# Kernel optimization log

Hardware: AMD Instinct MI355X
Metric: run time of the kernel (lower is better)

The kernel has to match this reference:

```python
import jax, jax.numpy as jnp
import numpy as np

N_NODES = 100000
IN_CH = 65
HID_CH = 64
N_EDGES = 3200000


def setup_inputs() -> dict:
    key = jax.random.key(0)
    k1, k2, k3, k4, k5 = jax.random.split(key, 5)
    x = jax.random.normal(k1, (N_NODES, IN_CH), dtype=jnp.float32)
    edge_index = jax.random.randint(k2, (2, N_EDGES), 0, N_NODES, dtype=jnp.int64)
    edge_weight = jax.random.uniform(k3, (N_EDGES,), dtype=jnp.float32)
    # PyG GraphConv params: lin_rel (with bias) applied to aggregated neighbors,
    # lin_root (no bias) applied to self features.
    scale = 1.0 / np.sqrt(IN_CH)
    W_rel = jax.random.uniform(k4, (HID_CH, IN_CH), dtype=jnp.float32, minval=-scale, maxval=scale)
    b_rel = jnp.zeros((HID_CH,), dtype=jnp.float32)
    W_root = jax.random.uniform(k5, (HID_CH, IN_CH), dtype=jnp.float32, minval=-scale, maxval=scale)
    return {"x": x, "edge_index": edge_index, "edge_weight": edge_weight,
            "W_rel": W_rel, "b_rel": b_rel, "W_root": W_root}


def reference(x, edge_index, edge_weight, W_rel, b_rel, W_root):
    src = edge_index[0]  # source nodes (x_j in PyG message)
    dst = edge_index[1]  # target nodes (aggregation index)
    # gather neighbor features, weight by edge weight: [E, IN_CH]
    msgs = x[src] * edge_weight[:, None]
    # scatter-add to destination nodes: [N, IN_CH]
    aggr = jax.ops.segment_sum(msgs, dst, num_segments=N_NODES)
    # out = lin_rel(aggr) + lin_root(x)
    out = aggr @ W_rel.T + b_rel + x @ W_root.T
    return out
```

## Files before the change

kernel.cpp:

```cpp
#include <hip/hip_runtime.h>

#define IN_CH 65
#define HID 64
#define BN 64
#define NB 1563
#define CAP 2560
#define SCAP 2432
#define EPB 12288
#define TPS 1024
#define EPT (EPB / TPS)
#define WSTR 132

static inline size_t align16(size_t v) { return (v + 15) & ~(size_t)15; }

__device__ inline ushort f2bf(float f) {
    uint u = __float_as_uint(f);
    return (ushort)((u + 0x7FFF + ((u >> 16) & 1)) >> 16);
}

__global__ __launch_bounds__(256) void k1both(const float* __restrict__ x,
                                              const float* __restrict__ W_rel,
                                              const float* __restrict__ W_root,
                                              const float* __restrict__ b_rel,
                                              ushort* __restrict__ y16,
                                              float* __restrict__ out,
                                              int* __restrict__ cnt, int nBuckets,
                                              int nNodes) {
    __shared__ float xsT[65 * 68];
    __shared__ float ws[65 * 68];
    const int tid = threadIdx.x;
    const int tx = tid & 15;
    const int ty = tid >> 4;
    const long nodeBase = (long)blockIdx.x * 64;
    const int nValid = (int)min((long)64, (long)nNodes - nodeBase);

    if (cnt && tid == 0 && blockIdx.x < (unsigned)nBuckets) cnt[blockIdx.x] = 0;

    for (int f = tid; f < HID * IN_CH; f += 256) {
        const int j = f / IN_CH, c = f - j * IN_CH;
        ws[c * 68 + j] = W_rel[f];
    }
    const float* xsrc = x + nodeBase * IN_CH;
    for (int f = tid; f < 64 * IN_CH; f += 256) {
        const int node = f / IN_CH, k = f - node * IN_CH;
        xsT[k * 68 + node] = (node < nValid) ? xsrc[f] : 0.f;
    }
    __syncthreads();

    const int r0 = ty * 4;
    const int c0 = tx * 4;

    {
        float acc[4][4];
#pragma unroll
        for (int i = 0; i < 4; ++i)
#pragma unroll
            for (int j = 0; j < 4; ++j) acc[i][j] = 0.f;

        for (int k = 0; k < IN_CH; ++k) {
            const float4 a4 = *(const float4*)&xsT[k * 68 + r0];
            const float4 b4 = *(const float4*)&ws[k * 68 + c0];
            const float aa[4] = {a4.x, a4.y, a4.z, a4.w};
            const float bb[4] = {b4.x, b4.y, b4.z, b4.w};
#pragma unroll
            for (int i = 0; i < 4; ++i)
#pragma unroll
                for (int j = 0; j < 4; ++j) acc[i][j] += aa[i] * bb[j];
        }
#pragma unroll
        for (int i = 0; i < 4; ++i) {
            const long node = nodeBase + r0 + i;
            if (node >= nNodes) break;
            uint2 pk;
            pk.x = (uint)f2bf(acc[i][0]) | ((uint)f2bf(acc[i][1]) << 16);
            pk.y = (uint)f2bf(acc[i][2]) | ((uint)f2bf(acc[i][3]) << 16);
            *(uint2*)&y16[node * HID + c0] = pk;
        }
    }
    __syncthreads();

    for (int f = tid; f < HID * IN_CH; f += 256) {
        const int j = f / IN_CH, c = f - j * IN_CH;
        ws[c * 68 + j] = W_root[f];
    }
    __syncthreads();

    {
        const float4 bb4 = *(const float4*)&b_rel[c0];
        float acc[4][4];
#pragma unroll
        for (int i = 0; i < 4; ++i) {
            acc[i][0] = bb4.x; acc[i][1] = bb4.y;
            acc[i][2] = bb4.z; acc[i][3] = bb4.w;
        }
        for (int k = 0; k < IN_CH; ++k) {
            const float4 a4 = *(const float4*)&xsT[k * 68 + r0];
            const float4 b4 = *(const float4*)&ws[k * 68 + c0];
            const float aa[4] = {a4.x, a4.y, a4.z, a4.w};
            const float bb[4] = {b4.x, b4.y, b4.z, b4.w};
#pragma unroll
            for (int i = 0; i < 4; ++i)
#pragma unroll
                for (int j = 0; j < 4; ++j) acc[i][j] += aa[i] * bb[j];
        }
#pragma unroll
        for (int i = 0; i < 4; ++i) {
            const long node = nodeBase + r0 + i;
            if (node >= nNodes) break;
            *(float4*)&out[node * HID + c0] =
                make_float4(acc[i][0], acc[i][1], acc[i][2], acc[i][3]);
        }
    }
}

__global__ __launch_bounds__(TPS) void scatterB(const int* __restrict__ ei,
                                                const float* __restrict__ ew,
                                                int* __restrict__ cnt,
                                                int2* __restrict__ pairs, int E) {
    __shared__ int lhist[NB];
    __shared__ int lbase[NB];
    const int tid = threadIdx.x;
    const long e0 = (long)blockIdx.x * EPB;
    const int n = (int)min((long)EPB, (long)E - e0);

    for (int i = tid; i < NB; i += TPS) lhist[i] = 0;
    __syncthreads();

    int dstv[EPT], srcv[EPT];
    float wv[EPT];
#pragma unroll
    for (int k = 0; k < EPT; ++k) {
        const int i = tid + k * TPS;
        const bool valid = i < n;
        dstv[k] = valid ? ei[(long)E + e0 + i] : 0;
        srcv[k] = valid ? ei[e0 + i] : 0;
        wv[k]   = valid ? ew[e0 + i] : 0.f;
        if (valid) atomicAdd(&lhist[dstv[k] >> 6], 1);
    }
    __syncthreads();

    for (int i = tid; i < NB; i += TPS) {
        const int c = lhist[i];
        lbase[i] = c ? atomicAdd(&cnt[i], c) : 0;
        lhist[i] = 0;
    }
    __syncthreads();

#pragma unroll
    for (int k = 0; k < EPT; ++k) {
        const int i = tid + k * TPS;
        if (i < n) {
            const int b = dstv[k] >> 6;
            const int p = lbase[b] + atomicAdd(&lhist[b], 1);
            if (p < CAP)
                pairs[(size_t)b * CAP + p] =
                    make_int2((srcv[k] << 7) | ((dstv[k] & (BN - 1)) << 25),
                              __float_as_int(wv[k]));
        }
    }
}

__global__ __launch_bounds__(512) void aggregateS16(const int2* __restrict__ pairs,
                                                    const int* __restrict__ cnt,
                                                    const ushort* __restrict__ y16,
                                                    float* __restrict__ out, int N) {
    __shared__ int2 sorted[SCAP];
    __shared__ int sH[BN];
    __shared__ int soff[BN + 1];
    __shared__ int scur[BN];
    const int tid = threadIdx.x;
    const int lane = tid & 63;
    const int wvid = tid >> 6;
    const int half = lane >> 5;
    const uint lane4 = (lane & 31) * 4;
    const int b = blockIdx.x;

    if (tid < BN) { sH[tid] = 0; scur[tid] = 0; }

    const int m = min(cnt[b], CAP);
    const int2* pb = pairs + (size_t)b * CAP;

    int2 pv[5];
#pragma unroll
    for (int kk = 0; kk < 5; ++kk) {
        const int i = tid + kk * 512;
        if (i < m) pv[kk] = pb[i];
    }
    __syncthreads();

#pragma unroll
    for (int kk = 0; kk < 5; ++kk) {
        const int i = tid + kk * 512;
        if (i < m) atomicAdd(&sH[(uint)pv[kk].x >> 25], 1);
    }
    __syncthreads();

    for (int off = 1; off < BN; off <<= 1) {
        int v = 0;
        if (tid < BN) {
            v = sH[tid];
            if (tid >= off) v += sH[tid - off];
        }
        __syncthreads();
        if (tid < BN) sH[tid] = v;
        __syncthreads();
    }
    if (tid < BN) soff[tid + 1] = sH[tid];
    if (tid == 0) soff[0] = 0;
    __syncthreads();

#pragma unroll
    for (int kk = 0; kk < 5; ++kk) {
        const int i = tid + kk * 512;
        if (i < m) {
            const int d = (uint)pv[kk].x >> 25;
            const int slot = soff[d] + atomicAdd(&scur[d], 1);
            if (slot < SCAP) sorted[slot] = make_int2(pv[kk].x & 0x00FFFF80, pv[kk].y);
        }
    }
    __syncthreads();

    const char* yb = (const char*)y16;
    const long nodeBase = (long)b * BN;
    for (int nl = wvid; nl < BN; nl += 8) {
        const long node = nodeBase + nl;
        if (node >= N) break;
        const int kbeg = min(soff[nl], SCAP);
        const int kend = min(soff[nl + 1], SCAP);
        float2* o = (float2*)(out + node * HID) + (lane & 31);
        const float2 cur = *o;
        float ax = 0.f, ay = 0.f;
        int k = kbeg + half;
        for (; k + 14 < kend; k += 16) {
            int2 pp[8];
#pragma unroll
            for (int j = 0; j < 8; ++j) pp[j] = sorted[k + 2 * j];
            uint qq[8];
#pragma unroll
            for (int j = 0; j < 8; ++j)
                qq[j] = *(const uint*)(yb + (uint)pp[j].x + lane4);
#pragma unroll
            for (int j = 0; j < 8; ++j) {
                const float w = __int_as_float(pp[j].y);
                ax += w * __uint_as_float(qq[j] << 16);
                ay += w * __uint_as_float(qq[j] & 0xFFFF0000u);
            }
        }
        for (; k + 6 < kend; k += 8) {
            const int2 p0 = sorted[k],     p1 = sorted[k + 2];
            const int2 p2 = sorted[k + 4], p3 = sorted[k + 6];
            const uint q0 = *(const uint*)(yb + (uint)p0.x + lane4);
            const uint q1 = *(const uint*)(yb + (uint)p1.x + lane4);
            const uint q2 = *(const uint*)(yb + (uint)p2.x + lane4);
            const uint q3 = *(const uint*)(yb + (uint)p3.x + lane4);
            const float w0 = __int_as_float(p0.y), w1 = __int_as_float(p1.y);
            const float w2 = __int_as_float(p2.y), w3 = __int_as_float(p3.y);
            ax += w0 * __uint_as_float(q0 << 16);
            ay += w0 * __uint_as_float(q0 & 0xFFFF0000u);
            ax += w1 * __uint_as_float(q1 << 16);
            ay += w1 * __uint_as_float(q1 & 0xFFFF0000u);
            ax += w2 * __uint_as_float(q2 << 16);
            ay += w2 * __uint_as_float(q2 & 0xFFFF0000u);
            ax += w3 * __uint_as_float(q3 << 16);
            ay += w3 * __uint_as_float(q3 & 0xFFFF0000u);
        }
        for (; k < kend; k += 2) {
            const int2 p = sorted[k];
            const uint q = *(const uint*)(yb + (uint)p.x + lane4);
            const float w = __int_as_float(p.y);
            ax += w * __uint_as_float(q << 16);
            ay += w * __uint_as_float(q & 0xFFFF0000u);
        }
        ax += __shfl_xor(ax, 32);
        ay += __shfl_xor(ay, 32);
        if (half == 0) {
            *o = make_float2(cur.x + ax, cur.y + ay);
        }
    }
}

__global__ __launch_bounds__(256) void k1_full(const float* __restrict__ x,
                                               const float* __restrict__ W_rel,
                                               const float* __restrict__ b_rel,
                                               const float* __restrict__ W_root,
                                               ushort* __restrict__ y16,
                                               float* __restrict__ out,
                                               int nNodes) {
    __shared__ float xs[64 * IN_CH];
    __shared__ float ws[IN_CH * WSTR];
    const int tid = threadIdx.x;
    const int tx = tid & 15;
    const int ty = tid >> 4;
    const long nodeBase = (long)blockIdx.x * 64;
    const int nValid = min(64, nNodes - (int)nodeBase);
    const int nx = nValid * IN_CH;

    for (int f = tid; f < HID * IN_CH; f += 256) {
        const int j = f / IN_CH, c = f - j * IN_CH;
        ws[c * WSTR + j] = W_rel[f];
    }
    for (int f = tid; f < HID * IN_CH; f += 256) {
        const int j = f / IN_CH, c = f - j * IN_CH;
        ws[c * WSTR + HID + j] = W_root[f];
    }
    const float* xsrc = x + nodeBase * IN_CH;
    for (int i = tid; i < 64 * IN_CH; i += 256) xs[i] = (i < nx) ? xsrc[i] : 0.f;
    __syncthreads();

    float acc[4][8];
#pragma unroll
    for (int i = 0; i < 4; ++i)
#pragma unroll
        for (int j = 0; j < 8; ++j) acc[i][j] = 0.f;

    const int r0 = ty * 4;
    const int c0 = tx * 8;
    for (int k = 0; k < IN_CH; ++k) {
        float aa[4] = {xs[(r0 + 0) * IN_CH + k], xs[(r0 + 1) * IN_CH + k],
                       xs[(r0 + 2) * IN_CH + k], xs[(r0 + 3) * IN_CH + k]};
        float4 b0 = *(const float4*)&ws[k * WSTR + c0];
        float4 b1 = *(const float4*)&ws[k * WSTR + c0 + 4];
        float bb[8] = {b0.x, b0.y, b0.z, b0.w, b1.x, b1.y, b1.z, b1.w};
#pragma unroll
        for (int i = 0; i < 4; ++i)
#pragma unroll
            for (int j = 0; j < 8; ++j) acc[i][j] += aa[i] * bb[j];
    }

    if (c0 >= HID) {
        const int h0 = c0 - HID;
        float4 bb0 = *(const float4*)&b_rel[h0];
        float4 bb1 = *(const float4*)&b_rel[h0 + 4];
        float bv[8] = {bb0.x, bb0.y, bb0.z, bb0.w, bb1.x, bb1.y, bb1.z, bb1.w};
#pragma unroll
        for (int i = 0; i < 4; ++i)
#pragma unroll
            for (int j = 0; j < 8; ++j) acc[i][j] += bv[j];
    }

#pragma unroll
    for (int i = 0; i < 4; ++i) {
        const long node = nodeBase + r0 + i;
        if (node >= nNodes) break;
        if (c0 < HID) {
            uint4 pk;
            pk.x = (uint)f2bf(acc[i][0]) | ((uint)f2bf(acc[i][1]) << 16);
            pk.y = (uint)f2bf(acc[i][2]) | ((uint)f2bf(acc[i][3]) << 16);
            pk.z = (uint)f2bf(acc[i][4]) | ((uint)f2bf(acc[i][5]) << 16);
            pk.w = (uint)f2bf(acc[i][6]) | ((uint)f2bf(acc[i][7]) << 16);
            *(uint4*)&y16[node * HID + c0] = pk;
        } else {
            float* dst = out + node * HID + (c0 - HID);
            *(float4*)(dst + 0) = make_float4(acc[i][0], acc[i][1], acc[i][2], acc[i][3]);
            *(float4*)(dst + 4) = make_float4(acc[i][4], acc[i][5], acc[i][6], acc[i][7]);
        }
    }
}

__global__ __launch_bounds__(256) void k2_atomic16(const int* __restrict__ ei,
                                                   const float* __restrict__ ew,
                                                   const ushort* __restrict__ y16,
                                                   float* __restrict__ out, int E) {
    const long t = (long)blockIdx.x * 256 + threadIdx.x;
    const long e = t >> 4;
    const int r = (int)(t & 15);
    if (e >= E) return;
    const int src = ei[e];
    const int dst = ei[(long)E + e];
    const float w = ew[e];
    const uint2 q = ((const uint2*)y16)[(size_t)src * 16 + r];
    float* o = out + (size_t)dst * HID + r * 4;
    unsafeAtomicAdd(o + 0, w * __uint_as_float(q.x << 16));
    unsafeAtomicAdd(o + 1, w * __uint_as_float(q.x & 0xFFFF0000u));
    unsafeAtomicAdd(o + 2, w * __uint_as_float(q.y << 16));
    unsafeAtomicAdd(o + 3, w * __uint_as_float(q.y & 0xFFFF0000u));
}

extern "C" void kernel_launch(void* const* d_in, const int* in_sizes, int n_in,
                              void* d_out, int out_size, void* d_ws, size_t ws_size,
                              hipStream_t stream) {
    const float* x      = (const float*)d_in[0];
    const int*   ei     = (const int*)d_in[1];
    const float* ew     = (const float*)d_in[2];
    const float* W_rel  = (const float*)d_in[3];
    const float* b_rel  = (const float*)d_in[4];
    const float* W_root = (const float*)d_in[5];
    float* out = (float*)d_out;

    const int N = in_sizes[0] / IN_CH;
    const int E = in_sizes[2];

    char* base = (char*)d_ws;
    const size_t oY     = 0;
    const size_t oPairs = align16((size_t)N * HID * 2);
    const size_t oCnt   = oPairs + align16((size_t)NB * CAP * 8);
    const size_t need   = oCnt + (size_t)NB * 4;

    ushort* y16 = (ushort*)(base + oY);
    const int nb1 = (N + 63) / 64;

    const bool fits = (ws_size >= need) && (N <= (1 << 17)) &&
                      ((size_t)NB * BN >= (size_t)N) && ((long)E <= (long)N * 33) &&
                      (nb1 >= NB);

    if (fits) {
        int2* pairs = (int2*)(base + oPairs);
        int*  cnt   = (int*)(base + oCnt);

        k1both<<<nb1, 256, 0, stream>>>(x, W_rel, W_root, b_rel, y16, out, cnt, NB, N);
        scatterB<<<(E + EPB - 1) / EPB, TPS, 0, stream>>>(ei, ew, cnt, pairs, E);
        aggregateS16<<<NB, 512, 0, stream>>>(pairs, cnt, y16, out, N);
    } else {
        const int nbf = (N + 63) / 64;
        k1_full<<<nbf, 256, 0, stream>>>(x, W_rel, b_rel, W_root, y16, out, N);
        const long thr2 = (long)E * 16;
        k2_atomic16<<<(int)((thr2 + 255) / 256), 256, 0, stream>>>(ei, ew, y16, out, E);
    }
}
```

Measured before the change: 238.9 us.

## Fuse dense GEMM and edge bucketing into one interleaved-role prep kernel

Replaces the separate node-GEMM kernel and edge-scatter kernel with a single launch. Block roles interleave two GEMM blocks (each handling two 64-node tiles with 256-thread halves) per one scatter block (8192 edges, 512 threads). The goal is to overlap the compute-bound dense transform with the memory- and atomic-bound bucketing and to drop one kernel boundary. Clearing the bucket counters moves to a hipMemsetAsync. The trade-off is large shared memory per block (about 70 KB), which limits occupancy, and more scatter blocks, which means more global atomics on the counters.

```diff
diff --git a/kernel.cpp b/kernel.cpp
--- a/kernel.cpp
+++ b/kernel.cpp
@@ -6,9 +6,10 @@
 #define NB 1563
 #define CAP 2560
 #define SCAP 2432
-#define EPB 12288
-#define TPS 1024
-#define EPT (EPB / TPS)
+#define GT 2
+#define PTPB 512
+#define SEPB 8192
+#define SEPT (SEPB / PTPB)
 #define WSTR 132
 
 static inline size_t align16(size_t v) { return (v + 15) & ~(size_t)15; }
@@ -18,144 +19,149 @@
     return (ushort)((u + 0x7FFF + ((u >> 16) & 1)) >> 16);
 }
 
-__global__ __launch_bounds__(256) void k1both(const float* __restrict__ x,
-                                              const float* __restrict__ W_rel,
-                                              const float* __restrict__ W_root,
-                                              const float* __restrict__ b_rel,
-                                              ushort* __restrict__ y16,
-                                              float* __restrict__ out,
-                                              int* __restrict__ cnt, int nBuckets,
-                                              int nNodes) {
-    __shared__ float xsT[65 * 68];
-    __shared__ float ws[65 * 68];
+__global__ __launch_bounds__(PTPB) void prep(const float* __restrict__ x,
+                                             const float* __restrict__ W_rel,
+                                             const float* __restrict__ W_root,
+                                             const float* __restrict__ b_rel,
+                                             ushort* __restrict__ y16,
+                                             float* __restrict__ out,
+                                             const int* __restrict__ ei,
+                                             const float* __restrict__ ew,
+                                             int* __restrict__ cnt,
+                                             int2* __restrict__ pairs,
+                                             int nNodes, int nTiles, int E) {
+    __shared__ __align__(16) char smem[4 * 65 * 68 * 4];
+    const int bid = blockIdx.x;
+    const int s3 = bid / 3, r3 = bid - s3 * 3;
     const int tid = threadIdx.x;
-    const int tx = tid & 15;
-    const int ty = tid >> 4;
-    const long nodeBase = (long)blockIdx.x * 64;
-    const int nValid = (int)min((long)64, (long)nNodes - nodeBase);
-
-    if (cnt && tid == 0 && blockIdx.x < (unsigned)nBuckets) cnt[blockIdx.x] = 0;
-
-    for (int f = tid; f < HID * IN_CH; f += 256) {
-        const int j = f / IN_CH, c = f - j * IN_CH;
-        ws[c * 68 + j] = W_rel[f];
-    }
-    const float* xsrc = x + nodeBase * IN_CH;
-    for (int f = tid; f < 64 * IN_CH; f += 256) {
-        const int node = f / IN_CH, k = f - node * IN_CH;
-        xsT[k * 68 + node] = (node < nValid) ? xsrc[f] : 0.f;
-    }
-    __syncthreads();
-
-    const int r0 = ty * 4;
-    const int c0 = tx * 4;
-
-    {
-        float acc[4][4];
-#pragma unroll
-        for (int i = 0; i < 4; ++i)
-#pragma unroll
-            for (int j = 0; j < 4; ++j) acc[i][j] = 0.f;
-
-        for (int k = 0; k < IN_CH; ++k) {
-            const float4 a4 = *(const float4*)&xsT[k * 68 + r0];
-            const float4 b4 = *(const float4*)&ws[k * 68 + c0];
-            const float aa[4] = {a4.x, a4.y, a4.z, a4.w};
-            const float bb[4] = {b4.x, b4.y, b4.z, b4.w};
+
+    if (r3 != 2) {
+        const int gblk = s3 * 2 + r3;
+        const int sub = tid >> 8;
+        const int t256 = tid & 255;
+        const int tile = gblk * GT + sub;
+        float* xsT = (float*)smem + sub * (65 * 68);
+        float* ws  = (float*)smem + (2 + sub) * (65 * 68);
+        const int tx = t256 & 15;
+        const int ty = t256 >> 4;
+        const long nodeBase = (long)tile * 64;
+        const int nValid = (int)min((long)64, (long)nNodes - nodeBase);
+
+        for (int f = t256; f < HID * IN_CH; f += 256) {
+            const int j = f / IN_CH, c = f - j * IN_CH;
+            ws[c * 68 + j] = W_rel[f];
+        }
+        const float* xsrc = x + nodeBase * IN_CH;
+        for (int f = t256; f < 64 * IN_CH; f += 256) {
+            const int node = f / IN_CH, k = f - node * IN_CH;
+            xsT[k * 68 + node] = (node < nValid) ? xsrc[f] : 0.f;
+        }
+        __syncthreads();
+
+        const int r0 = ty * 4;
+        const int c0 = tx * 4;
+
+        {
+            float acc[4][4];
 #pragma unroll
             for (int i = 0; i < 4; ++i)
 #pragma unroll
-                for (int j = 0; j < 4; ++j) acc[i][j] += aa[i] * bb[j];
-        }
-#pragma unroll
-        for (int i = 0; i < 4; ++i) {
-            const long node = nodeBase + r0 + i;
-            if (node >= nNodes) break;
-            uint2 pk;
-            pk.x = (uint)f2bf(acc[i][0]) | ((uint)f2bf(acc[i][1]) << 16);
-            pk.y = (uint)f2bf(acc[i][2]) | ((uint)f2bf(acc[i][3]) << 16);
-            *(uint2*)&y16[node * HID + c0] = pk;
-        }
-    }
-    __syncthreads();
-
-    for (int f = tid; f < HID * IN_CH; f += 256) {
-        const int j = f / IN_CH, c = f - j * IN_CH;
-        ws[c * 68 + j] = W_root[f];
-    }
-    __syncthreads();
-
-    {
-        const float4 bb4 = *(const float4*)&b_rel[c0];
-        float acc[4][4];
-#pragma unroll
-        for (int i = 0; i < 4; ++i) {
-            acc[i][0] = bb4.x; acc[i][1] = bb4.y;
-            acc[i][2] = bb4.z; acc[i][3] = bb4.w;
-        }
-        for (int k = 0; k < IN_CH; ++k) {
-            const float4 a4 = *(const float4*)&xsT[k * 68 + r0];
-            const float4 b4 = *(const float4*)&ws[k * 68 + c0];
-            const float aa[4] = {a4.x, a4.y, a4.z, a4.w};
-            const float bb[4] = {b4.x, b4.y, b4.z, b4.w};
-#pragma unroll
-            for (int i = 0; i < 4; ++i)
-#pragma unroll
-                for (int j = 0; j < 4; ++j) acc[i][j] += aa[i] * bb[j];
-        }
-#pragma unroll
-        for (int i = 0; i < 4; ++i) {
-            const long node = nodeBase + r0 + i;
-            if (node >= nNodes) break;
-            *(float4*)&out[node * HID + c0] =
-                make_float4(acc[i][0], acc[i][1], acc[i][2], acc[i][3]);
-        }
-    }
-}
-
-__global__ __launch_bounds__(TPS) void scatterB(const int* __restrict__ ei,
-                                                const float* __restrict__ ew,
-                                                int* __restrict__ cnt,
-                                                int2* __restrict__ pairs, int E) {
-    __shared__ int lhist[NB];
-    __shared__ int lbase[NB];
-    const int tid = threadIdx.x;
-    const long e0 = (long)blockIdx.x * EPB;
-    const int n = (int)min((long)EPB, (long)E - e0);
-
-    for (int i = tid; i < NB; i += TPS) lhist[i] = 0;
-    __syncthreads();
-
-    int dstv[EPT], srcv[EPT];
-    float wv[EPT];
-#pragma unroll
-    for (int k = 0; k < EPT; ++k) {
-        const int i = tid + k * TPS;
-        const bool valid = i < n;
-        dstv[k] = valid ? ei[(long)E + e0 + i] : 0;
-        srcv[k] = valid ? ei[e0 + i] : 0;
-        wv[k]   = valid ? ew[e0 + i] : 0.f;
-        if (valid) atomicAdd(&lhist[dstv[k] >> 6], 1);
-    }
-    __syncthreads();
-
-    for (int i = tid; i < NB; i += TPS) {
-        const int c = lhist[i];
-        lbase[i] = c ? atomicAdd(&cnt[i], c) : 0;
-        lhist[i] = 0;
-    }
-    __syncthreads();
-
-#pragma unroll
-    for (int k = 0; k < EPT; ++k) {
-        const int i = tid + k * TPS;
-        if (i < n) {
-            const int b = dstv[k] >> 6;
-            const int p = lbase[b] + atomicAdd(&lhist[b], 1);
-            if (p < CAP)
-                pairs[(size_t)b * CAP + p] =
-                    make_int2((srcv[k] << 7) | ((dstv[k] & (BN - 1)) << 25),
-                              __float_as_int(wv[k]));
+                for (int j = 0; j < 4; ++j) acc[i][j] = 0.f;
+
+            for (int k = 0; k < IN_CH; ++k) {
+                const float4 a4 = *(const float4*)&xsT[k * 68 + r0];
+                const float4 b4 = *(const float4*)&ws[k * 68 + c0];
+                const float aa[4] = {a4.x, a4.y, a4.z, a4.w};
+                const float bb[4] = {b4.x, b4.y, b4.z, b4.w};
+#pragma unroll
+                for (int i = 0; i < 4; ++i)
+#pragma unroll
+                    for (int j = 0; j < 4; ++j) acc[i][j] += aa[i] * bb[j];
+            }
+#pragma unroll
+            for (int i = 0; i < 4; ++i) {
+                const long node = nodeBase + r0 + i;
+                if (node >= nNodes) break;
+                uint2 pk;
+                pk.x = (uint)f2bf(acc[i][0]) | ((uint)f2bf(acc[i][1]) << 16);
+                pk.y = (uint)f2bf(acc[i][2]) | ((uint)f2bf(acc[i][3]) << 16);
+                *(uint2*)&y16[node * HID + c0] = pk;
+            }
+        }
+        __syncthreads();
+
+        for (int f = t256; f < HID * IN_CH; f += 256) {
+            const int j = f / IN_CH, c = f - j * IN_CH;
+            ws[c * 68 + j] = W_root[f];
+        }
+        __syncthreads();
+
+        {
+            const float4 bb4 = *(const float4*)&b_rel[c0];
+            float acc[4][4];
+#pragma unroll
+            for (int i = 0; i < 4; ++i) {
+                acc[i][0] = bb4.x; acc[i][1] = bb4.y;
+                acc[i][2] = bb4.z; acc[i][3] = bb4.w;
+            }
+            for (int k = 0; k < IN_CH; ++k) {
+                const float4 a4 = *(const float4*)&xsT[k * 68 + r0];
+                const float4 b4 = *(const float4*)&ws[k * 68 + c0];
+                const float aa[4] = {a4.x, a4.y, a4.z, a4.w};
+                const float bb[4] = {b4.x, b4.y, b4.z, b4.w};
+#pragma unroll
+                for (int i = 0; i < 4; ++i)
+#pragma unroll
+                    for (int j = 0; j < 4; ++j) acc[i][j] += aa[i] * bb[j];
+            }
+#pragma unroll
+            for (int i = 0; i < 4; ++i) {
+                const long node = nodeBase + r0 + i;
+                if (node >= nNodes) break;
+                *(float4*)&out[node * HID + c0] =
+                    make_float4(acc[i][0], acc[i][1], acc[i][2], acc[i][3]);
+            }
+        }
+    } else {
+        int* lhist = (int*)smem;
+        int* lbase = lhist + NB;
+        const long e0 = (long)s3 * SEPB;
+        const int n = (int)min((long)SEPB, (long)E - e0);
+
+        for (int i = tid; i < NB; i += PTPB) lhist[i] = 0;
+        __syncthreads();
+
+        int dstv[SEPT], srcv[SEPT];
+        float wv[SEPT];
+#pragma unroll
+        for (int k = 0; k < SEPT; ++k) {
+            const int i = tid + k * PTPB;
+            const bool valid = i < n;
+            dstv[k] = valid ? ei[(long)E + e0 + i] : 0;
+            srcv[k] = valid ? ei[e0 + i] : 0;
+            wv[k]   = valid ? ew[e0 + i] : 0.f;
+            if (valid) atomicAdd(&lhist[dstv[k] >> 6], 1);
+        }
+        __syncthreads();
+
+        for (int i = tid; i < NB; i += PTPB) {
+            const int c = lhist[i];
+            lbase[i] = c ? atomicAdd(&cnt[i], c) : 0;
+            lhist[i] = 0;
+        }
+        __syncthreads();
+
+#pragma unroll
+        for (int k = 0; k < SEPT; ++k) {
+            const int i = tid + k * PTPB;
+            if (i < n) {
+                const int b = dstv[k] >> 6;
+                const int p = lbase[b] + atomicAdd(&lhist[b], 1);
+                if (p < CAP)
+                    pairs[(size_t)b * CAP + p] =
+                        make_int2((srcv[k] << 7) | ((dstv[k] & (BN - 1)) << 25),
+                                  __float_as_int(wv[k]));
+            }
         }
     }
 }
@@ -397,18 +403,24 @@
     const size_t need   = oCnt + (size_t)NB * 4;
 
     ushort* y16 = (ushort*)(base + oY);
-    const int nb1 = (N + 63) / 64;
+    const int nTiles = (N + 63) / 64;
 
     const bool fits = (ws_size >= need) && (N <= (1 << 17)) &&
-                      ((size_t)NB * BN >= (size_t)N) && ((long)E <= (long)N * 33) &&
-                      (nb1 >= NB);
+                      ((size_t)NB * BN >= (size_t)N) && ((long)E <= (long)N * 33);
 
     if (fits) {
         int2* pairs = (int2*)(base + oPairs);
         int*  cnt   = (int*)(base + oCnt);
 
-        k1both<<<nb1, 256, 0, stream>>>(x, W_rel, W_root, b_rel, y16, out, cnt, NB, N);
-        scatterB<<<(E + EPB - 1) / EPB, TPS, 0, stream>>>(ei, ew, cnt, pairs, E);
+        hipMemsetAsync(cnt, 0, (size_t)NB * sizeof(int), stream);
+
+        const int gemmBlocks = (nTiles + GT - 1) / GT;
+        const int scatBlocks = (E + SEPB - 1) / SEPB;
+        const int nTrip = max((gemmBlocks + 1) / 2, scatBlocks);
+        const int grid = nTrip * 3;
+
+        prep<<<grid, PTPB, 0, stream>>>(x, W_rel, W_root, b_rel, y16, out,
+                                        ei, ew, cnt, pairs, N, nTiles, E);
         aggregateS16<<<NB, 512, 0, stream>>>(pairs, cnt, y16, out, N);
     } else {
         const int nbf = (N + 63) / 64;
```

Result: faster. 220.6 us (-7.7%).
